# Kernel optimization log

Hardware: AMD Instinct MI355X
Metric: run time of the kernel (lower is better)

Reference implementation:

```python
import jax, jax.numpy as jnp
import numpy as np

NUM_GRAPHS = 128
NODES_PER_GRAPH = 512
N_NODES = NUM_GRAPHS * NODES_PER_GRAPH
N_EDGES = 524288
IN_DIM = 128
HID = 128
OUT_DIM = 10
N_LAYERS = 3
POOL_RATIO = 0.5  # TopKPooling default ratio


def setup_inputs() -> dict:
    key = jax.random.key(0)
    ks = jax.random.split(key, 16)
    x = jax.random.normal(ks[0], (N_NODES, IN_DIM), dtype=jnp.float32)
    edge_index = jax.random.randint(ks[1], (2, N_EDGES), 0, N_NODES, dtype=jnp.int64)
    batch = jnp.repeat(jnp.arange(NUM_GRAPHS, dtype=jnp.int64), NODES_PER_GRAPH)
    s = 0.05
    return {
        "x": x,
        "edge_index": edge_index,
        "batch": batch,
        "emb_W": jax.random.normal(ks[2], (IN_DIM, HID), dtype=jnp.float32) * s,
        "emb_b": jnp.zeros((HID,), dtype=jnp.float32),
        "gcn_W": jax.random.normal(ks[3], (N_LAYERS, HID, HID), dtype=jnp.float32) * s,
        "gcn_b": jnp.zeros((N_LAYERS, HID), dtype=jnp.float32),
        "pool_p": jax.random.normal(ks[4], (HID,), dtype=jnp.float32),
        "fc1_W": jax.random.normal(ks[5], (HID, 128), dtype=jnp.float32) * s,
        "fc1_b": jnp.zeros((128,), dtype=jnp.float32),
        "fc2_W": jax.random.normal(ks[6], (128, 64), dtype=jnp.float32) * s,
        "fc2_b": jnp.zeros((64,), dtype=jnp.float32),
        "fc3_W": jax.random.normal(ks[7], (64, OUT_DIM), dtype=jnp.float32) * s,
        "fc3_b": jnp.zeros((OUT_DIM,), dtype=jnp.float32),
    }


def reference(x, edge_index, batch, emb_W, emb_b, gcn_W, gcn_b, pool_p,
              fc1_W, fc1_b, fc2_W, fc2_b, fc3_W, fc3_b):
    n = x.shape[0]
    # embedding
    h = x @ emb_W + emb_b
    # GCNConv normalization (PyG semantics): add self loops, deg from target scatter
    loop = jnp.arange(n, dtype=edge_index.dtype)
    src = jnp.concatenate([edge_index[0], loop])
    dst = jnp.concatenate([edge_index[1], loop])
    deg = jax.ops.segment_sum(jnp.ones_like(src, dtype=h.dtype), dst, num_segments=n)
    dinv = jnp.where(deg > 0, jax.lax.rsqrt(jnp.maximum(deg, 1e-12)), 0.0)
    norm = dinv[src] * dinv[dst]  # [E+n]
    for l in range(gcn_W.shape[0]):
        hw = h @ gcn_W[l]                                   # [n, HID]
        msg = hw[src] * norm[:, None]                        # gather + scale
        h = jax.nn.relu(jax.ops.segment_sum(msg, dst, num_segments=n) + gcn_b[l])
    # TopKPooling (ratio=0.5, tanh nonlinearity), uniform graphs -> reshape + top_k
    npg = n // NUM_GRAPHS
    k = int(np.ceil(POOL_RATIO * npg))
    score = (h @ pool_p) / jnp.linalg.norm(pool_p)           # [n]
    score_g = score.reshape(NUM_GRAPHS, npg)
    topv, topi = jax.lax.top_k(score_g, k)                   # [G, k]
    h_g = h.reshape(NUM_GRAPHS, npg, -1)
    h_sel = jnp.take_along_axis(h_g, topi[:, :, None], axis=1) * jnp.tanh(topv)[:, :, None]
    pooled = h_sel.mean(axis=1)                              # global_mean_pool -> [G, HID]
    # MLP head (dropout is identity in eval)
    z = jax.nn.relu(pooled @ fc1_W + fc1_b)
    z = jax.nn.relu(z @ fc2_W + fc2_b)
    return z @ fc3_W + fc3_b
```

## Files before the change

### kernel.cpp

```cpp
#include <hip/hip_runtime.h>
#include <hip/hip_bf16.h>
#include <math.h>


#define SLOTS 48

static __device__ __forceinline__ float4 f4add(float4 a, float4 b) {
    return make_float4(a.x + b.x, a.y + b.y, a.z + b.z, a.w + b.w);
}
static __device__ __forceinline__ float4 f4fma(float s, float4 a, float4 acc) {
    return make_float4(fmaf(s, a.x, acc.x), fmaf(s, a.y, acc.y),
                       fmaf(s, a.z, acc.z), fmaf(s, a.w, acc.w));
}

__global__ __launch_bounds__(256) void build_graph_fold(
    const int* __restrict__ src, const int* __restrict__ dst,
    int* __restrict__ cnt, int* __restrict__ csr_pad, int E, int EB,
    const float* __restrict__ embW, const float* __restrict__ embb,
    const float* __restrict__ W0, float* __restrict__ W01,
    float* __restrict__ b01, float* __restrict__ zrow)
{
    const int b = blockIdx.x;
    if (b < EB) {
        int e = b * 256 + threadIdx.x;
        if (e < E) {
            int d = dst[e];
            int r = atomicAdd(&cnt[d], 1);
            if (r < SLOTS) csr_pad[d * SLOTS + r] = src[e];
        }
        return;
    }
    __shared__ float rs[128];
    __shared__ float part[256];
    const int r = b - EB;
    const int t = threadIdx.x;
    if (r == 0 && t < 128) zrow[t] = 0.f;
    const int c = t & 127, q = t >> 7;
    if (t < 128) rs[t] = (r < 128) ? embW[r * 128 + t] : embb[t];
    __syncthreads();
    float s = 0.f;
    const int k0 = q * 64;
#pragma unroll 8
    for (int k = k0; k < k0 + 64; k++) s = fmaf(rs[k], W0[k * 128 + c], s);
    part[t] = s;
    __syncthreads();
    if (q == 0) {
        float v = part[c] + part[c + 128];
        if (r < 128) W01[r * 128 + c] = v;
        else         b01[c] = v;
    }
}

#define ASTRIDE 129
#define WSTRIDE 140
__global__ __launch_bounds__(256) void gemm128(
    const float* __restrict__ A, const float* __restrict__ W,
    const float* __restrict__ bias, const int* __restrict__ rowdeg,
    float* __restrict__ out, int n)
{
    __shared__ float As[32 * ASTRIDE];
    __shared__ float Ws[32 * WSTRIDE];
    const int tid  = threadIdx.x;
    const int rb   = blockIdx.x * 128;
    const int tc   = tid & 15;
    const int tr   = tid >> 4;
    const int colg = tc * 8;
    const int cswz = colg + ((colg >> 5) << 2);
    const int rowg = tr * 8;

    const int a_kq = tid & 7;
    const int a_m  = tid >> 3;
    const int w_c  = (tid & 31) * 4;
    const int w_cs = w_c + ((w_c >> 5) << 2);
    const int w_k  = tid >> 5;

    float acc[8][8];
#pragma unroll
    for (int i = 0; i < 8; i++)
#pragma unroll
        for (int j = 0; j < 8; j++) acc[i][j] = 0.f;

    float4 areg[4], wreg[4];
#pragma unroll
    for (int t = 0; t < 4; t++)
        areg[t] = *(const float4*)&A[(size_t)(rb + t * 32 + a_m) * 128 + a_kq * 4];
#pragma unroll
    for (int t = 0; t < 4; t++)
        wreg[t] = *(const float4*)&W[(size_t)(t * 8 + w_k) * 128 + w_c];

#pragma unroll 1
    for (int k0 = 0; k0 < 128; k0 += 32) {
#pragma unroll
        for (int t = 0; t < 4; t++) {
            const int m = t * 32 + a_m;
            const float4 av = areg[t];
            As[(a_kq * 4 + 0) * ASTRIDE + m] = av.x;
            As[(a_kq * 4 + 1) * ASTRIDE + m] = av.y;
            As[(a_kq * 4 + 2) * ASTRIDE + m] = av.z;
            As[(a_kq * 4 + 3) * ASTRIDE + m] = av.w;
        }
#pragma unroll
        for (int t = 0; t < 4; t++)
            *(float4*)&Ws[(t * 8 + w_k) * WSTRIDE + w_cs] = wreg[t];
        __syncthreads();
        if (k0 < 96) {
#pragma unroll
            for (int t = 0; t < 4; t++)
                areg[t] = *(const float4*)&A[(size_t)(rb + t * 32 + a_m) * 128 + k0 + 32 + a_kq * 4];
#pragma unroll
            for (int t = 0; t < 4; t++)
                wreg[t] = *(const float4*)&W[(size_t)(k0 + 32 + t * 8 + w_k) * 128 + w_c];
        }
#pragma unroll 8
        for (int kk = 0; kk < 32; kk++) {
            float4 a0 = *(const float4*)&As[kk * ASTRIDE + rowg];
            float4 a1 = *(const float4*)&As[kk * ASTRIDE + rowg + 4];
            float4 b0 = *(const float4*)&Ws[kk * WSTRIDE + cswz];
            float4 b1 = *(const float4*)&Ws[kk * WSTRIDE + cswz + 4];
            float av[8] = {a0.x, a0.y, a0.z, a0.w, a1.x, a1.y, a1.z, a1.w};
            float bv[8] = {b0.x, b0.y, b0.z, b0.w, b1.x, b1.y, b1.z, b1.w};
#pragma unroll
            for (int i = 0; i < 8; i++)
#pragma unroll
                for (int j = 0; j < 8; j++) acc[i][j] = fmaf(av[i], bv[j], acc[i][j]);
        }
        __syncthreads();
    }

    float4 bb0 = make_float4(0.f, 0.f, 0.f, 0.f), bb1 = bb0;
    if (bias) {
        bb0 = *(const float4*)&bias[colg];
        bb1 = *(const float4*)&bias[colg + 4];
    }
#pragma unroll
    for (int i = 0; i < 8; i++) {
        const int row  = rb + rowg + i;
        const float sc = rowdeg ? rsqrtf((float)(rowdeg[row] + 1)) : 1.f;
        float4 o0, o1;
        o0.x = (acc[i][0] + bb0.x) * sc;  o0.y = (acc[i][1] + bb0.y) * sc;
        o0.z = (acc[i][2] + bb0.z) * sc;  o0.w = (acc[i][3] + bb0.w) * sc;
        o1.x = (acc[i][4] + bb1.x) * sc;  o1.y = (acc[i][5] + bb1.y) * sc;
        o1.z = (acc[i][6] + bb1.z) * sc;  o1.w = (acc[i][7] + bb1.w) * sc;
        *(float4*)&out[(size_t)row * 128 + colg]     = o0;
        *(float4*)&out[(size_t)row * 128 + colg + 4] = o1;
    }
}

__global__ __launch_bounds__(256) void aggregate(
    const float* __restrict__ hs, const int* __restrict__ csr_pad,
    const int* __restrict__ cnt, const float* __restrict__ bias,
    float* __restrict__ hout,
    const float* __restrict__ pool_p, float* __restrict__ scores, int n)
{
    const int grp  = threadIdx.x >> 5;
    const int lane = threadIdx.x & 31;
    const int node = blockIdx.x * 8 + grp;
    const float4* __restrict__ hv = (const float4*)hs;

    const int deg = cnt[node];
    const int e0  = node * SLOTS;

    int4 c4[4];
#pragma unroll
    for (int q = 0; q < 4; q++)
        c4[q] = *(const int4*)&csr_pad[e0 + q * 4];
    int ix[16] = {c4[0].x, c4[0].y, c4[0].z, c4[0].w,
                  c4[1].x, c4[1].y, c4[1].z, c4[1].w,
                  c4[2].x, c4[2].y, c4[2].z, c4[2].w,
                  c4[3].x, c4[3].y, c4[3].z, c4[3].w};
#pragma unroll
    for (int j = 0; j < 16; j++)
        ix[j] = (j < deg) ? ix[j] : n;

    float4 self = hv[(size_t)node * 32 + lane];
    float4 r[16];
#pragma unroll
    for (int j = 0; j < 16; j++)
        r[j] = hv[(size_t)ix[j] * 32 + lane];
    asm volatile("" ::: "memory");

    float4 a0 = self;
    float4 a1 = make_float4(0.f, 0.f, 0.f, 0.f);
    float4 a2 = a1, a3 = a1;
#pragma unroll
    for (int j = 0; j < 16; j += 4) {
        a0 = f4add(a0, r[j + 0]);
        a1 = f4add(a1, r[j + 1]);
        a2 = f4add(a2, r[j + 2]);
        a3 = f4add(a3, r[j + 3]);
    }
    const int dcap = deg < SLOTS ? deg : SLOTS;
    for (int j = 16; j < dcap; j++) {
        a1 = f4add(a1, hv[(size_t)csr_pad[e0 + j] * 32 + lane]);
    }

    float4 s = f4add(f4add(a0, a1), f4add(a2, a3));
    const float dv = rsqrtf((float)(deg + 1));
    const float4 bb = ((const float4*)bias)[lane];
    float4 o;
    o.x = fmaxf(fmaf(s.x, dv, bb.x), 0.f);
    o.y = fmaxf(fmaf(s.y, dv, bb.y), 0.f);
    o.z = fmaxf(fmaf(s.z, dv, bb.z), 0.f);
    o.w = fmaxf(fmaf(s.w, dv, bb.w), 0.f);
    ((float4*)hout)[(size_t)node * 32 + lane] = o;

    if (scores) {
        float4 pv = ((const float4*)pool_p)[lane];
        float d  = o.x * pv.x + o.y * pv.y + o.z * pv.z + o.w * pv.w;
        float nn = pv.x * pv.x + pv.y * pv.y + pv.z * pv.z + pv.w * pv.w;
#pragma unroll
        for (int off = 16; off > 0; off >>= 1) {
            d  += __shfl_xor(d, off);
            nn += __shfl_xor(nn, off);
        }
        if (lane == 0) scores[node] = d * rsqrtf(nn);
    }
}

__global__ __launch_bounds__(512) void topk_mlp(
    const float* __restrict__ scores, const float* __restrict__ h,
    const float* __restrict__ fc1W, const float* __restrict__ fc1b,
    const float* __restrict__ fc2W, const float* __restrict__ fc2b,
    const float* __restrict__ fc3W, const float* __restrict__ fc3b,
    float* __restrict__ out)
{
    __shared__ float s[512];
    __shared__ int   sel[256];
    __shared__ float w[256];
    __shared__ float4 red[512];
    __shared__ float pld[128];
    __shared__ float z1[128];
    __shared__ float z2[64];
    const int g = blockIdx.x;
    const int i = threadIdx.x;
    s[i] = scores[g * 512 + i];
    __syncthreads();
    float si = s[i];
    int rank = 0;
    for (int j = 0; j < 512; j++) {
        float sj = s[j];
        rank += (sj > si) || (sj == si && j < i);
    }
    if (rank < 256) {
        sel[rank] = i;
        w[rank]   = tanhf(si) * (1.f / 256.f);
    }
    __syncthreads();
    const int c   = (i & 31) * 4;
    const int grp = i >> 5;
    float4 acc = make_float4(0.f, 0.f, 0.f, 0.f);
    for (int t = grp; t < 256; t += 16) {
        float wt  = w[t];
        int   idx = sel[t];
        float4 r = *(const float4*)&h[((size_t)g * 512 + idx) * 128 + c];
        acc = f4fma(wt, r, acc);
    }
    red[i] = acc;
    __syncthreads();
    if (i < 256) red[i] = f4add(red[i], red[i + 256]);
    __syncthreads();
    if (i < 128) red[i] = f4add(red[i], red[i + 128]);
    __syncthreads();
    if (i < 64) red[i] = f4add(red[i], red[i + 64]);
    __syncthreads();
    if (i < 32) {
        float4 v = f4add(red[i], red[i + 32]);
        *(float4*)&pld[i * 4] = v;
    }
    __syncthreads();
    if (i < 128) {
        float a = fc1b[i];
        for (int k = 0; k < 128; k++) a += pld[k] * fc1W[k * 128 + i];
        z1[i] = fmaxf(a, 0.f);
    }
    __syncthreads();
    if (i < 64) {
        float b = fc2b[i];
        for (int k = 0; k < 128; k++) b += z1[k] * fc2W[k * 64 + i];
        z2[i] = fmaxf(b, 0.f);
    }
    __syncthreads();
    if (i < 10) {
        float o = fc3b[i];
        for (int k = 0; k < 64; k++) o += z2[k] * fc3W[k * 10 + i];
        out[g * 10 + i] = o;
    }
}

extern "C" void kernel_launch(void* const* d_in, const int* in_sizes, int n_in,
                              void* d_out, int out_size, void* d_ws, size_t ws_size,
                              hipStream_t stream)
{
    const float* x     = (const float*)d_in[0];
    const int*   eidx  = (const int*)d_in[1];
    const float* embW  = (const float*)d_in[3];
    const float* embb  = (const float*)d_in[4];
    const float* gcnW  = (const float*)d_in[5];
    const float* gcnb  = (const float*)d_in[6];
    const float* poolp = (const float*)d_in[7];
    const float* fc1W  = (const float*)d_in[8];
    const float* fc1b  = (const float*)d_in[9];
    const float* fc2W  = (const float*)d_in[10];
    const float* fc2b  = (const float*)d_in[11];
    const float* fc3W  = (const float*)d_in[12];
    const float* fc3b  = (const float*)d_in[13];
    float* out = (float*)d_out;

    const int n = in_sizes[0] / 128;
    const int E = in_sizes[1] / 2;
    const int G = n / 512;

    const int* src = eidx;
    const int* dst = eidx + E;

    char* ws = (char*)d_ws;
    size_t off = 0;
    auto carve = [&](size_t bytes) {
        void* p = ws + off;
        off += (bytes + 255) & ~(size_t)255;
        return p;
    };
    float* h       = (float*)carve((size_t)n * 128 * 4);
    float* hs      = (float*)carve((size_t)(n + 1) * 128 * 4);
    int*   cnt     = (int*)carve((size_t)n * 4);
    int*   csr_pad = (int*)carve((size_t)n * SLOTS * 4);
    float* scores  = (float*)carve((size_t)n * 4);
    float* W01     = (float*)carve(128 * 128 * 4);
    float* b01     = (float*)carve(128 * 4);
    (void)ws_size;

    const int EB = E / 256;

    hipMemsetAsync(cnt, 0, (size_t)n * 4, stream);
    build_graph_fold<<<EB + 129, 256, 0, stream>>>(
        src, dst, cnt, csr_pad, E, EB, embW, embb, gcnW, W01, b01,
        hs + (size_t)n * 128);

    gemm128<<<n / 128, 256, 0, stream>>>(x, W01, b01, cnt, hs, n);
    aggregate<<<n / 8, 256, 0, stream>>>(hs, csr_pad, cnt, gcnb, h,
                                         poolp, nullptr, n);

    for (int l = 1; l < 3; l++) {
        gemm128<<<n / 128, 256, 0, stream>>>(h, gcnW + (size_t)l * 128 * 128,
                                             nullptr, cnt, hs, n);
        aggregate<<<n / 8, 256, 0, stream>>>(
            hs, csr_pad, cnt, gcnb + (size_t)l * 128, h,
            poolp, (l == 2) ? scores : nullptr, n);
    }

    topk_mlp<<<G, 512, 0, stream>>>(scores, h, fc1W, fc1b, fc2W, fc2b,
                                    fc3W, fc3b, out);
}
```

Baseline: 401.9 us.

## Fuse GCN aggregation with next layer's GEMM in one kernel

Adds an agg_gemm kernel that gathers neighbor rows for a 128-node tile, applies normalization, bias and ReLU, writes the result into shared memory as the A operand, and multiplies by the next layer's weight in the same block. This replaces two aggregate+gemm pairs with two fused launches and ping-pongs between two scaled-feature buffers, so the intermediate h never goes to global memory. The cost is only 512 blocks with large shared memory and register use, which lowers occupancy and latency hiding for the irregular gathers.

```diff
diff --git a/kernel.cpp b/kernel.cpp
--- a/kernel.cpp
+++ b/kernel.cpp
@@ -18,7 +18,8 @@
     int* __restrict__ cnt, int* __restrict__ csr_pad, int E, int EB,
     const float* __restrict__ embW, const float* __restrict__ embb,
     const float* __restrict__ W0, float* __restrict__ W01,
-    float* __restrict__ b01, float* __restrict__ zrow)
+    float* __restrict__ b01, float* __restrict__ zrowA,
+    float* __restrict__ zrowB)
 {
     const int b = blockIdx.x;
     if (b < EB) {
@@ -34,7 +35,7 @@
     __shared__ float part[256];
     const int r = b - EB;
     const int t = threadIdx.x;
-    if (r == 0 && t < 128) zrow[t] = 0.f;
+    if (r == 0 && t < 128) { zrowA[t] = 0.f; zrowB[t] = 0.f; }
     const int c = t & 127, q = t >> 7;
     if (t < 128) rs[t] = (r < 128) ? embW[r * 128 + t] : embb[t];
     __syncthreads();
@@ -143,6 +144,144 @@
         o1.z = (acc[i][6] + bb1.z) * sc;  o1.w = (acc[i][7] + bb1.w) * sc;
         *(float4*)&out[(size_t)row * 128 + colg]     = o0;
         *(float4*)&out[(size_t)row * 128 + colg + 4] = o1;
+    }
+}
+
+__global__ __launch_bounds__(256) void agg_gemm(
+    const float* __restrict__ hs_in, const int* __restrict__ csr_pad,
+    const int* __restrict__ cnt, const float* __restrict__ aggb,
+    const float* __restrict__ W, float* __restrict__ hs_out, int n)
+{
+    __shared__ int   s_idx[128 * 17];
+    __shared__ float s_dinv[128];
+    __shared__ int   s_deg[128];
+    __shared__ float As[32 * ASTRIDE];
+    __shared__ float Ws[32 * WSTRIDE];
+
+    const int tid = threadIdx.x;
+    const int rb  = blockIdx.x * 128;
+    const float4* __restrict__ hv = (const float4*)hs_in;
+
+    if (tid < 128) {
+        int d = cnt[rb + tid];
+        s_deg[tid]  = d;
+        s_dinv[tid] = rsqrtf((float)(d + 1));
+    }
+    {
+        const int m    = tid >> 1;
+        const int hf   = (tid & 1) * 8;
+        const int node = rb + m;
+        const int4 cA = *(const int4*)&csr_pad[node * SLOTS + hf];
+        const int4 cB = *(const int4*)&csr_pad[node * SLOTS + hf + 4];
+        const int  d  = cnt[node];
+        int* row = &s_idx[m * 17 + hf];
+        row[0] = (hf + 0 < d) ? cA.x : n;
+        row[1] = (hf + 1 < d) ? cA.y : n;
+        row[2] = (hf + 2 < d) ? cA.z : n;
+        row[3] = (hf + 3 < d) ? cA.w : n;
+        row[4] = (hf + 4 < d) ? cB.x : n;
+        row[5] = (hf + 5 < d) ? cB.y : n;
+        row[6] = (hf + 6 < d) ? cB.z : n;
+        row[7] = (hf + 7 < d) ? cB.w : n;
+    }
+    __syncthreads();
+
+    const int tc   = tid & 15;
+    const int tr   = tid >> 4;
+    const int colg = tc * 8;
+    const int cswz = colg + ((colg >> 5) << 2);
+    const int rowg = tr * 8;
+    const int w_c  = (tid & 31) * 4;
+    const int w_cs = w_c + ((w_c >> 5) << 2);
+    const int w_k  = tid >> 5;
+    const int ln = tid & 7;
+    const int nd = tid >> 3;
+
+    float acc[8][8];
+#pragma unroll
+    for (int i = 0; i < 8; i++)
+#pragma unroll
+        for (int j = 0; j < 8; j++) acc[i][j] = 0.f;
+
+#pragma unroll 1
+    for (int p = 0; p < 4; p++) {
+        float4 wreg[4];
+#pragma unroll
+        for (int t = 0; t < 4; t++)
+            wreg[t] = *(const float4*)&W[(size_t)(p * 32 + t * 8 + w_k) * 128 + w_c];
+
+        const int fo = p * 8 + ln;
+        const float4 bb = *(const float4*)&aggb[p * 32 + ln * 4];
+#pragma unroll 1
+        for (int ps = 0; ps < 4; ps++) {
+            const int m    = ps * 32 + nd;
+            const int node = rb + m;
+            const int* rowI = &s_idx[m * 17];
+            float4 self = hv[(size_t)node * 32 + fo];
+            float4 r[16];
+#pragma unroll
+            for (int j = 0; j < 16; j++)
+                r[j] = hv[(size_t)rowI[j] * 32 + fo];
+            asm volatile("" ::: "memory");
+            float4 a0 = self;
+            float4 a1 = make_float4(0.f, 0.f, 0.f, 0.f);
+            float4 a2 = a1, a3 = a1;
+#pragma unroll
+            for (int j = 0; j < 16; j += 4) {
+                a0 = f4add(a0, r[j + 0]);
+                a1 = f4add(a1, r[j + 1]);
+                a2 = f4add(a2, r[j + 2]);
+                a3 = f4add(a3, r[j + 3]);
+            }
+            const int d    = s_deg[m];
+            const int dcap = d < SLOTS ? d : SLOTS;
+            for (int j = 16; j < dcap; j++)
+                a1 = f4add(a1, hv[(size_t)csr_pad[node * SLOTS + j] * 32 + fo]);
+            float4 s = f4add(f4add(a0, a1), f4add(a2, a3));
+            const float dv = s_dinv[m];
+            float4 o;
+            o.x = fmaxf(fmaf(s.x, dv, bb.x), 0.f);
+            o.y = fmaxf(fmaf(s.y, dv, bb.y), 0.f);
+            o.z = fmaxf(fmaf(s.z, dv, bb.z), 0.f);
+            o.w = fmaxf(fmaf(s.w, dv, bb.w), 0.f);
+            const int kb = ln * 4;
+            As[(kb + 0) * ASTRIDE + m] = o.x;
+            As[(kb + 1) * ASTRIDE + m] = o.y;
+            As[(kb + 2) * ASTRIDE + m] = o.z;
+            As[(kb + 3) * ASTRIDE + m] = o.w;
+        }
+#pragma unroll
+        for (int t = 0; t < 4; t++)
+            *(float4*)&Ws[(t * 8 + w_k) * WSTRIDE + w_cs] = wreg[t];
+        __syncthreads();
+
+#pragma unroll 8
+        for (int kk = 0; kk < 32; kk++) {
+            float4 a0 = *(const float4*)&As[kk * ASTRIDE + rowg];
+            float4 a1 = *(const float4*)&As[kk * ASTRIDE + rowg + 4];
+            float4 b0 = *(const float4*)&Ws[kk * WSTRIDE + cswz];
+            float4 b1 = *(const float4*)&Ws[kk * WSTRIDE + cswz + 4];
+            float av[8] = {a0.x, a0.y, a0.z, a0.w, a1.x, a1.y, a1.z, a1.w};
+            float bv[8] = {b0.x, b0.y, b0.z, b0.w, b1.x, b1.y, b1.z, b1.w};
+#pragma unroll
+            for (int i = 0; i < 8; i++)
+#pragma unroll
+                for (int j = 0; j < 8; j++) acc[i][j] = fmaf(av[i], bv[j], acc[i][j]);
+        }
+        __syncthreads();
+    }
+
+#pragma unroll
+    for (int i = 0; i < 8; i++) {
+        const int row  = rb + rowg + i;
+        const float sc = s_dinv[rowg + i];
+        float4 o0, o1;
+        o0.x = acc[i][0] * sc;  o0.y = acc[i][1] * sc;
+        o0.z = acc[i][2] * sc;  o0.w = acc[i][3] * sc;
+        o1.x = acc[i][4] * sc;  o1.y = acc[i][5] * sc;
+        o1.z = acc[i][6] * sc;  o1.w = acc[i][7] * sc;
+        *(float4*)&hs_out[(size_t)row * 128 + colg]     = o0;
+        *(float4*)&hs_out[(size_t)row * 128 + colg + 4] = o1;
     }
 }
 
@@ -321,7 +460,8 @@
         return p;
     };
     float* h       = (float*)carve((size_t)n * 128 * 4);
-    float* hs      = (float*)carve((size_t)(n + 1) * 128 * 4);
+    float* hsA     = (float*)carve((size_t)(n + 1) * 128 * 4);
+    float* hsB     = (float*)carve((size_t)(n + 1) * 128 * 4);
     int*   cnt     = (int*)carve((size_t)n * 4);
     int*   csr_pad = (int*)carve((size_t)n * SLOTS * 4);
     float* scores  = (float*)carve((size_t)n * 4);
@@ -334,19 +474,17 @@
     hipMemsetAsync(cnt, 0, (size_t)n * 4, stream);
     build_graph_fold<<<EB + 129, 256, 0, stream>>>(
         src, dst, cnt, csr_pad, E, EB, embW, embb, gcnW, W01, b01,
-        hs + (size_t)n * 128);
-
-    gemm128<<<n / 128, 256, 0, stream>>>(x, W01, b01, cnt, hs, n);
-    aggregate<<<n / 8, 256, 0, stream>>>(hs, csr_pad, cnt, gcnb, h,
-                                         poolp, nullptr, n);
-
-    for (int l = 1; l < 3; l++) {
-        gemm128<<<n / 128, 256, 0, stream>>>(h, gcnW + (size_t)l * 128 * 128,
-                                             nullptr, cnt, hs, n);
-        aggregate<<<n / 8, 256, 0, stream>>>(
-            hs, csr_pad, cnt, gcnb + (size_t)l * 128, h,
-            poolp, (l == 2) ? scores : nullptr, n);
-    }
+        hsA + (size_t)n * 128, hsB + (size_t)n * 128);
+
+    gemm128<<<n / 128, 256, 0, stream>>>(x, W01, b01, cnt, hsA, n);
+
+    agg_gemm<<<n / 128, 256, 0, stream>>>(hsA, csr_pad, cnt, gcnb,
+                                          gcnW + (size_t)1 * 128 * 128, hsB, n);
+    agg_gemm<<<n / 128, 256, 0, stream>>>(hsB, csr_pad, cnt, gcnb + 128,
+                                          gcnW + (size_t)2 * 128 * 128, hsA, n);
+
+    aggregate<<<n / 8, 256, 0, stream>>>(hsA, csr_pad, cnt, gcnb + 256, h,
+                                         poolp, scores, n);
 
     topk_mlp<<<G, 512, 0, stream>>>(scores, h, fc1W, fc1b, fc2W, fc2b,
                                     fc3W, fc3b, out);
```

Result: faster. 353.5 us (-12.1%).
